# Kernel tuning notes

Hardware: AMD Instinct MI355X
Metric: run time of the kernel (lower is better)

The kernel has to match this reference:

```python
import jax, jax.numpy as jnp
import numpy as np

B, SQ, HIDDEN = 2, 2048, 2048
HEADS, GROUPS, KVC = 16, 4, 128
HPG = HEADS // GROUPS          # heads per group
LAYER_INDEX = 1
SCALE = KVC ** -0.5            # attention_softmax_scale_power = 0.5


def setup_inputs() -> dict:
    key = jax.random.key(0)
    k1, k2, k3, k4 = jax.random.split(key, 4)
    return {
        "x": jax.random.normal(k1, (B, SQ, HIDDEN), jnp.float32),
        "w_q": jax.random.normal(k2, (HIDDEN, HEADS * KVC), jnp.float32) * 0.02,
        "w_kv": jax.random.normal(k3, (HIDDEN, 2 * GROUPS * KVC), jnp.float32) * 0.02,
        "w_dense": jax.random.normal(k4, (HEADS * KVC, HIDDEN), jnp.float32) * 0.02,
    }


def reference(x, w_q, w_kv, w_dense):
    b, sq, _ = x.shape
    sk = sq
    # QKV projections
    q = jnp.einsum("bsh,he->bse", x, w_q).reshape(b, sq, GROUPS, HPG, KVC)
    kv = jnp.einsum("bsh,he->bse", x, w_kv)
    k, v = jnp.split(kv, 2, axis=-1)
    k = k.reshape(b, sk, GROUPS, KVC)
    v = v.reshape(b, sk, GROUPS, KVC)
    # scaled QK^T with the per-layer scale trick: alpha = scale/L in input
    # dtype, then cast to fp32 and multiply by L (as in _attn_fused)
    scores = jnp.einsum("bqgpd,bkgd->bgqpk", q, k) * (SCALE / LAYER_INDEX)
    scores = scores.astype(jnp.float32) * LAYER_INDEX
    # causal mask: mask = ~triu(ones, diagonal=1) -> keep where q_idx >= k_idx
    causal = (jnp.arange(sq)[:, None] >= jnp.arange(sk)[None, :])
    scores = jnp.where(causal[None, None, :, None, :], scores, -jnp.inf)
    probs = jax.nn.softmax(scores, axis=-1).astype(x.dtype)
    # dropout p = 0.0 -> no-op
    ctx = jnp.einsum("bgqpk,bkgd->bqgpd", probs, v).reshape(b, sq, HEADS * KVC)
    return jnp.einsum("bse,eh->bsh", ctx, w_dense)
```

## Files before the change

kernel.cpp:

```cpp
#include <hip/hip_runtime.h>
#include <hip/hip_bf16.h>


typedef __attribute__((ext_vector_type(4))) float f32x4;
typedef __attribute__((ext_vector_type(8))) short bf16x8;
typedef __attribute__((ext_vector_type(4))) short bf16x4;

__device__ __forceinline__ unsigned short f2bf(float f) {
    unsigned u = __builtin_bit_cast(unsigned, f);
    unsigned r = u + 0x7fffu + ((u >> 16) & 1u);
    return (unsigned short)(r >> 16);
}

__device__ __forceinline__ unsigned cvtpk_bf16(float lo, float hi) {
    unsigned r;
    asm("v_cvt_pk_bf16_f32 %0, %1, %2" : "=v"(r) : "v"(lo), "v"(hi));
    return r;
}

__device__ __forceinline__ void gl_lds16(const void* g, void* l) {
    __builtin_amdgcn_global_load_lds(
        (const __attribute__((address_space(1))) unsigned int*)g,
        (__attribute__((address_space(3))) unsigned int*)l, 16, 0, 0);
}

__device__ __forceinline__ int xcd_swizzle(int lin, int nwg) {
    return (lin & 7) * (nwg >> 3) + (lin >> 3);
}

__device__ __forceinline__ void xcvt_body(const float* __restrict__ in,
                                          unsigned short* __restrict__ out,
                                          int blk)
{
    size_t i = ((size_t)blk * 256 + threadIdx.x) * 8;
    float4 a = *reinterpret_cast<const float4*>(&in[i]);
    float4 b = *reinterpret_cast<const float4*>(&in[i + 4]);
    bf16x8 o = { (short)f2bf(a.x), (short)f2bf(a.y),
                 (short)f2bf(a.z), (short)f2bf(a.w),
                 (short)f2bf(b.x), (short)f2bf(b.y),
                 (short)f2bf(b.z), (short)f2bf(b.w) };
    *reinterpret_cast<bf16x8*>(&out[i]) = o;
}

__device__ __forceinline__ void wtrans_body(const float* __restrict__ in,
                                            unsigned short* __restrict__ out,
                                            int K, int N, int bx, int by,
                                            unsigned short* T)
{
    const int n0 = bx * 64, k0 = by * 64;
    const int tid = threadIdx.x;
#pragma unroll
    for (int i = 0; i < 4; ++i) {
        int f = tid + i * 256;
        int r = f >> 4;
        int c4 = (f & 15) * 4;
        float4 v = *reinterpret_cast<const float4*>(&in[(size_t)(k0 + r) * N + n0 + c4]);
        bf16x4 pk = { (short)f2bf(v.x), (short)f2bf(v.y),
                      (short)f2bf(v.z), (short)f2bf(v.w) };
        *reinterpret_cast<bf16x4*>(&T[r * 72 + c4]) = pk;
    }
    __syncthreads();
#pragma unroll
    for (int i = 0; i < 2; ++i) {
        int f = tid + i * 256;
        int nn = f >> 3;
        int s8 = (f & 7) * 8;
        bf16x8 o;
#pragma unroll
        for (int j = 0; j < 8; ++j) o[j] = T[(s8 + j) * 72 + nn];
        *reinterpret_cast<bf16x8*>(&out[(size_t)(n0 + nn) * K + k0 + s8]) = o;
    }
}

__device__ __forceinline__ void vtrans_body(const unsigned short* __restrict__ kv,
                                            unsigned short* __restrict__ vt,
                                            int bx, int bg, unsigned short* T)
{
    const int b = bg >> 2, g = bg & 3;
    const int s0 = bx * 64;
    const int tid = threadIdx.x;
#pragma unroll
    for (int i = 0; i < 4; ++i) {
        int f = tid + i * 256;
        int sl = f >> 4;
        int d0 = (f & 15) * 8;
        bf16x8 v = *reinterpret_cast<const bf16x8*>(
            &kv[(size_t)(b * 2048 + s0 + sl) * 1024 + 512 + g * 128 + d0]);
        bf16x4 lo = { v[0], v[1], v[2], v[3] };
        bf16x4 hi = { v[4], v[5], v[6], v[7] };
        *reinterpret_cast<bf16x4*>(&T[sl * 140 + d0])     = lo;
        *reinterpret_cast<bf16x4*>(&T[sl * 140 + d0 + 4]) = hi;
    }
    __syncthreads();
#pragma unroll
    for (int i = 0; i < 4; ++i) {
        int f = tid + i * 256;
        int d = f >> 3;
        int s8 = (f & 7) * 8;
        bf16x8 o;
#pragma unroll
        for (int j = 0; j < 8; ++j) o[j] = T[(s8 + j) * 140 + d];
        *reinterpret_cast<bf16x8*>(
            &vt[(size_t)(bg * 128 + d) * 2048 + s0 + s8]) = o;
    }
}

__global__ __launch_bounds__(256)
void prep1_kernel(const float* __restrict__ x, unsigned short* __restrict__ xbf,
                  const float* __restrict__ w_q, unsigned short* __restrict__ wqT,
                  const float* __restrict__ w_kv, unsigned short* __restrict__ wkvT)
{
    __shared__ __align__(16) unsigned short T[64 * 72];
    const int bid = blockIdx.x;
    if (bid < 4096) {
        xcvt_body(x, xbf, bid);
    } else if (bid < 4096 + 1024) {
        int r = bid - 4096;
        wtrans_body(w_q, wqT, 2048, 2048, r & 31, r >> 5, T);
    } else {
        int r = bid - 5120;
        wtrans_body(w_kv, wkvT, 2048, 1024, r & 15, r >> 4, T);
    }
}

__global__ __launch_bounds__(256)
void prep2_kernel(const float* __restrict__ w_dense, unsigned short* __restrict__ wdT,
                  const unsigned short* __restrict__ kv, unsigned short* __restrict__ vt)
{
    __shared__ __align__(16) unsigned short T[64 * 140];
    const int bid = blockIdx.x;
    if (bid < 1024) {
        wtrans_body(w_dense, wdT, 2048, 2048, bid & 31, bid >> 5, T);
    } else {
        int r = bid - 1024;
        vtrans_body(kv, vt, r & 31, r >> 5, T);
    }
}

__global__ __launch_bounds__(256)
void gemm_qkv_kernel(const unsigned short* __restrict__ A,
                     const unsigned short* __restrict__ BT,
                     void* __restrict__ C0v, void* __restrict__ C1v,
                     int M, int N, int K)
{
    __shared__ __align__(16) unsigned short Alds[3][128 * 32];
    __shared__ __align__(16) unsigned short Blds[3][128 * 32];

    const int tid = threadIdx.x;
    const int lane = tid & 63;
    const int wid = tid >> 6;
    const int wr = wid >> 1, wc = wid & 1;
    const int nbx = gridDim.x;
    const int lin = blockIdx.y * nbx + blockIdx.x;
    const int sl = xcd_swizzle(lin, nbx * gridDim.y);
    const int m0 = (sl / nbx) * 128;
    const int n0 = (sl % nbx) * 128;
    const int l16 = lane & 15, lg = lane >> 4;

    f32x4 acc[4][4];
#pragma unroll
    for (int m = 0; m < 4; ++m)
#pragma unroll
        for (int n = 0; n < 4; ++n) acc[m][n] = (f32x4){0.f, 0.f, 0.f, 0.f};

    int srow[2], skb[2];
#pragma unroll
    for (int i = 0; i < 2; ++i) {
        int L = i * 4096 + tid * 16;
        int R = L >> 7, c = L & 127;
        int cp = c ^ ((R & 7) << 4);
        srow[i] = 2 * R + (cp >> 6);
        skb[i]  = cp & 63;
    }

    auto stage = [&](int kt, int bi) {
#pragma unroll
        for (int i = 0; i < 2; ++i) {
            int L = i * 4096 + tid * 16;
            gl_lds16((const char*)A + ((size_t)(m0 + srow[i]) * K + kt) * 2 + skb[i],
                     (char*)(&Alds[bi][0]) + L);
            gl_lds16((const char*)BT + ((size_t)(n0 + srow[i]) * K + kt) * 2 + skb[i],
                     (char*)(&Blds[bi][0]) + L);
        }
    };

    const int NK = K / 32;
    stage(0, 0);
    stage(32, 1);

    for (int t = 0; t < NK; ++t) {
        const int bi = t % 3;
        if (t + 2 < NK) {
            stage((t + 2) * 32, (t + 2) % 3);
            asm volatile("s_waitcnt vmcnt(8)" ::: "memory");
        } else if (t + 1 < NK) {
            asm volatile("s_waitcnt vmcnt(4)" ::: "memory");
        } else {
            asm volatile("s_waitcnt vmcnt(0)" ::: "memory");
        }
        __builtin_amdgcn_s_barrier();

        const char* Ab = (const char*)(&Alds[bi][0]);
        const char* Bb = (const char*)(&Blds[bi][0]);

        bf16x8 af[4], bf[4];
#pragma unroll
        for (int m = 0; m < 4; ++m) {
            int row = wr * 64 + m * 16 + l16;
            int byte = (row >> 1) * 128 +
                       ((((row & 1) << 6) + lg * 16) ^ (((row >> 1) & 7) << 4));
            af[m] = *reinterpret_cast<const bf16x8*>(Ab + byte);
        }
#pragma unroll
        for (int n = 0; n < 4; ++n) {
            int row = wc * 64 + n * 16 + l16;
            int byte = (row >> 1) * 128 +
                       ((((row & 1) << 6) + lg * 16) ^ (((row >> 1) & 7) << 4));
            bf[n] = *reinterpret_cast<const bf16x8*>(Bb + byte);
        }
#pragma unroll
        for (int m = 0; m < 4; ++m)
#pragma unroll
            for (int n = 0; n < 4; ++n)
                acc[m][n] = __builtin_amdgcn_mfma_f32_16x16x32_bf16(
                    af[m], bf[n], acc[m][n], 0, 0, 0);

        __builtin_amdgcn_s_barrier();
    }

#pragma unroll
    for (int m = 0; m < 4; ++m) {
#pragma unroll
        for (int n = 0; n < 4; ++n) {
#pragma unroll
            for (int r = 0; r < 4; ++r) {
                int row = m0 + wr * 64 + m * 16 + lg * 4 + r;
                int col = n0 + wc * 64 + n * 16 + l16;
                float val = acc[m][n][r];
                if (n0 < 2048)
                    ((unsigned short*)C0v)[(size_t)row * 2048 + col] =
                        f2bf(val * 0.12751879523209208f);
                else
                    ((unsigned short*)C1v)[(size_t)row * 1024 + (col - 2048)] = f2bf(val);
            }
        }
    }
}

__global__ __launch_bounds__(256)
void gemm_dense_kernel(const unsigned short* __restrict__ A,
                       const unsigned short* __restrict__ BT,
                       float* __restrict__ C, int M, int N, int K)
{
    __shared__ __align__(16) unsigned short Alds[2][128 * 64];
    __shared__ __align__(16) unsigned short Blds[2][128 * 64];

    const int tid = threadIdx.x;
    const int lane = tid & 63;
    const int wid = tid >> 6;
    const int wr = wid >> 1, wc = wid & 1;
    const int nbx = gridDim.x;
    const int lin = blockIdx.y * nbx + blockIdx.x;
    const int sl = xcd_swizzle(lin, nbx * gridDim.y);
    const int m0 = (sl / nbx) * 128;
    const int n0 = (sl % nbx) * 128;
    const int l16 = lane & 15, lg = lane >> 4;

    f32x4 acc[4][4];
#pragma unroll
    for (int m = 0; m < 4; ++m)
#pragma unroll
        for (int n = 0; n < 4; ++n) acc[m][n] = (f32x4){0.f, 0.f, 0.f, 0.f};

    auto stage = [&](int kt, int bi) {
#pragma unroll
        for (int i = 0; i < 4; ++i) {
            int row = i * 32 + (tid >> 3);
            int cb = ((tid & 7) * 16) ^ ((row & 7) << 4);
            gl_lds16((const char*)A + ((size_t)(m0 + row) * K + kt) * 2 + cb,
                     (char*)(&Alds[bi][0]) + i * 4096 + wid * 1024);
            gl_lds16((const char*)BT + ((size_t)(n0 + row) * K + kt) * 2 + cb,
                     (char*)(&Blds[bi][0]) + i * 4096 + wid * 1024);
        }
    };

    const int NK = K / 64;
    stage(0, 0);
    int cur = 0;

    for (int kti = 0; kti < NK; ++kti) {
        if (kti + 1 < NK) {
            stage((kti + 1) * 64, cur ^ 1);
            asm volatile("s_waitcnt vmcnt(8)" ::: "memory");
        } else {
            asm volatile("s_waitcnt vmcnt(0)" ::: "memory");
        }
        __builtin_amdgcn_s_barrier();

        const char* Ab = (const char*)(&Alds[cur][0]);
        const char* Bb = (const char*)(&Blds[cur][0]);

        bf16x8 af[2][4], bf[2][4];
#pragma unroll
        for (int kd = 0; kd < 2; ++kd) {
#pragma unroll
            for (int m = 0; m < 4; ++m) {
                int row = wr * 64 + m * 16 + l16;
                af[kd][m] = *reinterpret_cast<const bf16x8*>(
                    Ab + row * 128 + ((kd * 64 + lg * 16) ^ ((row & 7) << 4)));
            }
#pragma unroll
            for (int n = 0; n < 4; ++n) {
                int row = wc * 64 + n * 16 + l16;
                bf[kd][n] = *reinterpret_cast<const bf16x8*>(
                    Bb + row * 128 + ((kd * 64 + lg * 16) ^ ((row & 7) << 4)));
            }
        }
#pragma unroll
        for (int kd = 0; kd < 2; ++kd)
#pragma unroll
            for (int m = 0; m < 4; ++m)
#pragma unroll
                for (int n = 0; n < 4; ++n)
                    acc[m][n] = __builtin_amdgcn_mfma_f32_16x16x32_bf16(
                        af[kd][m], bf[kd][n], acc[m][n], 0, 0, 0);

        __builtin_amdgcn_s_barrier();
        cur ^= 1;
    }

#pragma unroll
    for (int m = 0; m < 4; ++m) {
#pragma unroll
        for (int n = 0; n < 4; ++n) {
#pragma unroll
            for (int r = 0; r < 4; ++r) {
                int row = m0 + wr * 64 + m * 16 + lg * 4 + r;
                int col = n0 + wc * 64 + n * 16 + l16;
                C[(size_t)row * N + col] = acc[m][n][r];
            }
        }
    }
}

__global__ __launch_bounds__(256)
void attn_kernel(const unsigned short* __restrict__ Q,
                 const unsigned short* __restrict__ KV,
                 const unsigned short* __restrict__ VT,
                 unsigned short* __restrict__ CTX)
{
    constexpr int SQ = 2048;
    __shared__ __align__(16) unsigned short Klds[2][64 * 128];
    __shared__ __align__(16) unsigned short Vlds[2][128 * 64];
    __shared__ __align__(16) unsigned short Pl[4][16][64];

    const int tid = threadIdx.x;
    const int lane = tid & 63;
    const int w = tid >> 6;
    const int l16 = lane & 15, lg = lane >> 4;

    const int bid = blockIdx.x;
    const int gb = bid & 7;
    const int g = gb & 3, b = gb >> 2;
    const int pi = bid >> 3;
    const int hh = g * 4 + w;

    const size_t qbase = (size_t)b * SQ * 2048;
    const char* KVb = (const char*)KV + (size_t)b * SQ * 2048;
    const char* VTb = (const char*)VT;

    const int pswz = (l16 & 7) << 3;

    auto stage = [&](int t, int bi) {
        const int k0 = t * 64;
#pragma unroll
        for (int i = 0; i < 4; ++i) {
            int row = w * 16 + i * 4 + (lane >> 4);
            int scol = ((lane & 15) * 16) ^ ((row & 7) << 4);
            gl_lds16(KVb + (size_t)(k0 + row) * 2048 + g * 256 + scol,
                     (char*)(&Klds[bi][0]) + w * 4096 + i * 1024);
        }
#pragma unroll
        for (int i = 0; i < 4; ++i) {
            int row = w * 32 + i * 8 + (lane >> 3);
            int scol = ((lane & 7) * 16) ^ ((row & 7) << 4);
            gl_lds16(VTb + ((size_t)(gb * 128 + row) * 2048 + k0) * 2 + scol,
                     (char*)(&Vlds[bi][0]) + w * 4096 + i * 1024);
        }
    };

#pragma unroll 1
    for (int seg = 0; seg < 2; ++seg) {
        const int qt = seg ? pi : (127 - pi);
        const int ntiles = qt / 4 + 1;

        bf16x8 qfrag[4];
#pragma unroll
        for (int kd = 0; kd < 4; ++kd)
            qfrag[kd] = *reinterpret_cast<const bf16x8*>(
                &Q[qbase + (size_t)(qt * 16 + l16) * 2048 + hh * 128 + kd * 32 + lg * 8]);

        float lsum = 0.f;
        f32x4 acc[8];
#pragma unroll
        for (int nd = 0; nd < 8; ++nd) acc[nd] = (f32x4){0.f,0.f,0.f,0.f};

        stage(0, 0);

        for (int t = 0; t < ntiles; ++t) {
            const int bi = t & 1;
            const int k0 = t * 64;
            if (t + 1 < ntiles) {
                stage(t + 1, bi ^ 1);
                asm volatile("s_waitcnt vmcnt(8)" ::: "memory");
            } else {
                asm volatile("s_waitcnt vmcnt(0)" ::: "memory");
            }
            __builtin_amdgcn_s_barrier();

            const char* Kb = (const char*)(&Klds[bi][0]);
            const char* Vb = (const char*)(&Vlds[bi][0]);

            f32x4 st[4];
#pragma unroll
            for (int nf = 0; nf < 4; ++nf) st[nf] = (f32x4){0.f,0.f,0.f,0.f};
            __builtin_amdgcn_s_setprio(1);
#pragma unroll
            for (int nf = 0; nf < 4; ++nf) {
                int row = nf * 16 + l16;
#pragma unroll
                for (int kd = 0; kd < 4; ++kd) {
                    bf16x8 kf = *reinterpret_cast<const bf16x8*>(
                        Kb + row * 256 + ((kd * 64 + lg * 16) ^ ((row & 7) << 4)));
                    st[nf] = __builtin_amdgcn_mfma_f32_16x16x32_bf16(
                        kf, qfrag[kd], st[nf], 0, 0, 0);
                }
            }
            __builtin_amdgcn_s_setprio(0);

            const bool diag = (t == ntiles - 1);
            {
                float lacc = 0.f;
                const int q = qt * 16 + l16;
#pragma unroll
                for (int nf = 0; nf < 4; ++nf) {
                    float cs0 = st[nf][0];
                    float cs1 = st[nf][1];
                    float cs2 = st[nf][2];
                    float cs3 = st[nf][3];
                    if (diag) {
                        const int keyb = k0 + nf * 16 + lg * 4;
                        if (keyb + 0 > q) cs0 = -INFINITY;
                        if (keyb + 1 > q) cs1 = -INFINITY;
                        if (keyb + 2 > q) cs2 = -INFINITY;
                        if (keyb + 3 > q) cs3 = -INFINITY;
                    }
                    float p0 = exp2f(cs0), p1 = exp2f(cs1);
                    float p2 = exp2f(cs2), p3 = exp2f(cs3);
                    lacc += (p0 + p1) + (p2 + p3);
                    uint2 pk = { cvtpk_bf16(p0, p1), cvtpk_bf16(p2, p3) };
                    *reinterpret_cast<uint2*>(
                        &Pl[w][l16][(nf * 16 + lg * 4) ^ pswz]) = pk;
                }
                lacc += __shfl_xor(lacc, 16, 64);
                lacc += __shfl_xor(lacc, 32, 64);
                lsum += lacc;
            }

            __builtin_amdgcn_s_setprio(1);
#pragma unroll
            for (int kc = 0; kc < 2; ++kc) {
                bf16x8 pf = *reinterpret_cast<const bf16x8*>(
                    &Pl[w][l16][(kc * 32 + lg * 8) ^ pswz]);
#pragma unroll
                for (int nd = 0; nd < 8; ++nd) {
                    int row = nd * 16 + l16;
                    bf16x8 vf = *reinterpret_cast<const bf16x8*>(
                        Vb + row * 128 + ((kc * 64 + lg * 16) ^ ((row & 7) << 4)));
                    acc[nd] = __builtin_amdgcn_mfma_f32_16x16x32_bf16(
                        vf, pf, acc[nd], 0, 0, 0);
                }
            }
            __builtin_amdgcn_s_setprio(0);
            __builtin_amdgcn_s_barrier();
        }

        {
            float inv = 1.0f / lsum;
            const int q = qt * 16 + l16;
#pragma unroll
            for (int nd = 0; nd < 8; ++nd) {
                bf16x4 o = { (short)f2bf(acc[nd][0] * inv),
                             (short)f2bf(acc[nd][1] * inv),
                             (short)f2bf(acc[nd][2] * inv),
                             (short)f2bf(acc[nd][3] * inv) };
                *reinterpret_cast<bf16x4*>(
                    &CTX[qbase + (size_t)q * 2048 + hh * 128 + nd * 16 + lg * 4]) = o;
            }
        }
    }
}

extern "C" void kernel_launch(void* const* d_in, const int* in_sizes, int n_in,
                              void* d_out, int out_size, void* d_ws, size_t ws_size,
                              hipStream_t stream)
{
    const float* x       = (const float*)d_in[0];
    const float* w_q     = (const float*)d_in[1];
    const float* w_kv    = (const float*)d_in[2];
    const float* w_dense = (const float*)d_in[3];

    const int M = 4096;

    char* ws = (char*)d_ws;
    unsigned short* kv_buf  = (unsigned short*)(ws);
    unsigned short* ctx_buf = (unsigned short*)(ws + (8u << 20));
    unsigned short* wqT     = (unsigned short*)(ws + (24u << 20));
    unsigned short* wkvT    = (unsigned short*)(ws + (32u << 20));
    unsigned short* wdT     = wqT;
    unsigned short* xbf    = (unsigned short*)d_out;
    unsigned short* q_buf  = (unsigned short*)d_out + (size_t)M * 2048;
    unsigned short* vt_buf = (unsigned short*)d_out;

    dim3 blk(256);
    prep1_kernel<<<dim3(5632), blk, 0, stream>>>(x, xbf, w_q, wqT, w_kv, wkvT);
    gemm_qkv_kernel<<<dim3(24, 32), blk, 0, stream>>>(
        xbf, wqT, (void*)q_buf, (void*)kv_buf, M, 3072, 2048);
    prep2_kernel<<<dim3(1280), blk, 0, stream>>>(w_dense, wdT, kv_buf, vt_buf);
    attn_kernel<<<dim3(512), blk, 0, stream>>>(q_buf, kv_buf, vt_buf, ctx_buf);
    gemm_dense_kernel<<<dim3(16, 32), blk, 0, stream>>>(
        ctx_buf, wdT, (float*)d_out, M, 2048, 2048);
}
```

Baseline: 183.3 us.

## Repartition attention work: each wave owns a key slice across all four group heads

Warps now split keys and head dims instead of heads. Each wave computes scores for its 16-key slice across all 4 heads of the group, so every K fragment read from LDS feeds 4 MFMAs. Each wave then does P·V for its 32-column slice of V across all heads, through a shared P buffer. This cuts LDS traffic for K and V fragments. In exchange it adds an extra block barrier per tile, more Q registers, and a cross-wave LDS reduction of the row sums at the end.

```diff
diff --git a/kernel.cpp b/kernel.cpp
--- a/kernel.cpp
+++ b/kernel.cpp
@@ -352,7 +352,7 @@
     constexpr int SQ = 2048;
     __shared__ __align__(16) unsigned short Klds[2][64 * 128];
     __shared__ __align__(16) unsigned short Vlds[2][128 * 64];
-    __shared__ __align__(16) unsigned short Pl[4][16][64];
+    __shared__ __align__(16) unsigned short Pl[64][64];
 
     const int tid = threadIdx.x;
     const int lane = tid & 63;
@@ -363,13 +363,13 @@
     const int gb = bid & 7;
     const int g = gb & 3, b = gb >> 2;
     const int pi = bid >> 3;
-    const int hh = g * 4 + w;
 
     const size_t qbase = (size_t)b * SQ * 2048;
     const char* KVb = (const char*)KV + (size_t)b * SQ * 2048;
     const char* VTb = (const char*)VT;
 
-    const int pswz = (l16 & 7) << 3;
+    const int rsw = (l16 & 7) << 4;
+    float* Sred = reinterpret_cast<float*>(&Pl[0][0]);
 
     auto stage = [&](int t, int bi) {
         const int k0 = t * 64;
@@ -393,17 +393,23 @@
     for (int seg = 0; seg < 2; ++seg) {
         const int qt = seg ? pi : (127 - pi);
         const int ntiles = qt / 4 + 1;
-
-        bf16x8 qfrag[4];
-#pragma unroll
-        for (int kd = 0; kd < 4; ++kd)
-            qfrag[kd] = *reinterpret_cast<const bf16x8*>(
-                &Q[qbase + (size_t)(qt * 16 + l16) * 2048 + hh * 128 + kd * 32 + lg * 8]);
-
-        float lsum = 0.f;
-        f32x4 acc[8];
-#pragma unroll
-        for (int nd = 0; nd < 8; ++nd) acc[nd] = (f32x4){0.f,0.f,0.f,0.f};
+        const int q = qt * 16 + l16;
+
+        bf16x8 qfrag[4][4];
+#pragma unroll
+        for (int h = 0; h < 4; ++h)
+#pragma unroll
+            for (int kd = 0; kd < 4; ++kd)
+                qfrag[h][kd] = *reinterpret_cast<const bf16x8*>(
+                    &Q[qbase + (size_t)q * 2048 + (g * 4 + h) * 128 + kd * 32 + lg * 8]);
+
+        float part[4] = {0.f, 0.f, 0.f, 0.f};
+        f32x4 acc[4][2];
+#pragma unroll
+        for (int h = 0; h < 4; ++h) {
+            acc[h][0] = (f32x4){0.f,0.f,0.f,0.f};
+            acc[h][1] = (f32x4){0.f,0.f,0.f,0.f};
+        }
 
         stage(0, 0);
 
@@ -423,79 +429,85 @@
 
             f32x4 st[4];
 #pragma unroll
-            for (int nf = 0; nf < 4; ++nf) st[nf] = (f32x4){0.f,0.f,0.f,0.f};
+            for (int h = 0; h < 4; ++h) st[h] = (f32x4){0.f,0.f,0.f,0.f};
             __builtin_amdgcn_s_setprio(1);
 #pragma unroll
-            for (int nf = 0; nf < 4; ++nf) {
-                int row = nf * 16 + l16;
-#pragma unroll
-                for (int kd = 0; kd < 4; ++kd) {
-                    bf16x8 kf = *reinterpret_cast<const bf16x8*>(
-                        Kb + row * 256 + ((kd * 64 + lg * 16) ^ ((row & 7) << 4)));
-                    st[nf] = __builtin_amdgcn_mfma_f32_16x16x32_bf16(
-                        kf, qfrag[kd], st[nf], 0, 0, 0);
+            for (int kd = 0; kd < 4; ++kd) {
+                bf16x8 kf = *reinterpret_cast<const bf16x8*>(
+                    Kb + (w * 16 + l16) * 256 + ((kd * 64 + lg * 16) ^ rsw));
+#pragma unroll
+                for (int h = 0; h < 4; ++h)
+                    st[h] = __builtin_amdgcn_mfma_f32_16x16x32_bf16(
+                        kf, qfrag[h][kd], st[h], 0, 0, 0);
+            }
+            __builtin_amdgcn_s_setprio(0);
+
+            const bool diag = (t == ntiles - 1);
+            const int keyb = k0 + w * 16 + lg * 4;
+#pragma unroll
+            for (int h = 0; h < 4; ++h) {
+                float cs0 = st[h][0], cs1 = st[h][1];
+                float cs2 = st[h][2], cs3 = st[h][3];
+                if (diag) {
+                    if (keyb + 0 > q) cs0 = -INFINITY;
+                    if (keyb + 1 > q) cs1 = -INFINITY;
+                    if (keyb + 2 > q) cs2 = -INFINITY;
+                    if (keyb + 3 > q) cs3 = -INFINITY;
                 }
-            }
-            __builtin_amdgcn_s_setprio(0);
-
-            const bool diag = (t == ntiles - 1);
-            {
-                float lacc = 0.f;
-                const int q = qt * 16 + l16;
-#pragma unroll
-                for (int nf = 0; nf < 4; ++nf) {
-                    float cs0 = st[nf][0];
-                    float cs1 = st[nf][1];
-                    float cs2 = st[nf][2];
-                    float cs3 = st[nf][3];
-                    if (diag) {
-                        const int keyb = k0 + nf * 16 + lg * 4;
-                        if (keyb + 0 > q) cs0 = -INFINITY;
-                        if (keyb + 1 > q) cs1 = -INFINITY;
-                        if (keyb + 2 > q) cs2 = -INFINITY;
-                        if (keyb + 3 > q) cs3 = -INFINITY;
-                    }
-                    float p0 = exp2f(cs0), p1 = exp2f(cs1);
-                    float p2 = exp2f(cs2), p3 = exp2f(cs3);
-                    lacc += (p0 + p1) + (p2 + p3);
-                    uint2 pk = { cvtpk_bf16(p0, p1), cvtpk_bf16(p2, p3) };
-                    *reinterpret_cast<uint2*>(
-                        &Pl[w][l16][(nf * 16 + lg * 4) ^ pswz]) = pk;
-                }
-                lacc += __shfl_xor(lacc, 16, 64);
-                lacc += __shfl_xor(lacc, 32, 64);
-                lsum += lacc;
-            }
+                float p0 = exp2f(cs0), p1 = exp2f(cs1);
+                float p2 = exp2f(cs2), p3 = exp2f(cs3);
+                part[h] += (p0 + p1) + (p2 + p3);
+                uint2 pk = { cvtpk_bf16(p0, p1), cvtpk_bf16(p2, p3) };
+                *reinterpret_cast<uint2*>(
+                    (char*)&Pl[h * 16 + l16][0] + ((w * 32 + lg * 8) ^ rsw)) = pk;
+            }
+            asm volatile("s_waitcnt lgkmcnt(0)" ::: "memory");
+            __builtin_amdgcn_s_barrier();
 
             __builtin_amdgcn_s_setprio(1);
 #pragma unroll
             for (int kc = 0; kc < 2; ++kc) {
-                bf16x8 pf = *reinterpret_cast<const bf16x8*>(
-                    &Pl[w][l16][(kc * 32 + lg * 8) ^ pswz]);
-#pragma unroll
-                for (int nd = 0; nd < 8; ++nd) {
-                    int row = nd * 16 + l16;
-                    bf16x8 vf = *reinterpret_cast<const bf16x8*>(
-                        Vb + row * 128 + ((kc * 64 + lg * 16) ^ ((row & 7) << 4)));
-                    acc[nd] = __builtin_amdgcn_mfma_f32_16x16x32_bf16(
-                        vf, pf, acc[nd], 0, 0, 0);
+                bf16x8 vf0 = *reinterpret_cast<const bf16x8*>(
+                    Vb + (w * 32 + l16) * 128 + ((kc * 64 + lg * 16) ^ rsw));
+                bf16x8 vf1 = *reinterpret_cast<const bf16x8*>(
+                    Vb + (w * 32 + 16 + l16) * 128 + ((kc * 64 + lg * 16) ^ rsw));
+#pragma unroll
+                for (int h = 0; h < 4; ++h) {
+                    bf16x8 pf = *reinterpret_cast<const bf16x8*>(
+                        (const char*)&Pl[h * 16 + l16][0] + ((kc * 64 + lg * 16) ^ rsw));
+                    acc[h][0] = __builtin_amdgcn_mfma_f32_16x16x32_bf16(
+                        vf0, pf, acc[h][0], 0, 0, 0);
+                    acc[h][1] = __builtin_amdgcn_mfma_f32_16x16x32_bf16(
+                        vf1, pf, acc[h][1], 0, 0, 0);
                 }
             }
             __builtin_amdgcn_s_setprio(0);
             __builtin_amdgcn_s_barrier();
         }
 
-        {
-            float inv = 1.0f / lsum;
-            const int q = qt * 16 + l16;
-#pragma unroll
-            for (int nd = 0; nd < 8; ++nd) {
-                bf16x4 o = { (short)f2bf(acc[nd][0] * inv),
-                             (short)f2bf(acc[nd][1] * inv),
-                             (short)f2bf(acc[nd][2] * inv),
-                             (short)f2bf(acc[nd][3] * inv) };
+#pragma unroll
+        for (int h = 0; h < 4; ++h) {
+            part[h] += __shfl_xor(part[h], 16, 64);
+            part[h] += __shfl_xor(part[h], 32, 64);
+            Sred[(w * 4 + h) * 16 + l16] = part[h];
+        }
+        asm volatile("s_waitcnt lgkmcnt(0)" ::: "memory");
+        __builtin_amdgcn_s_barrier();
+
+#pragma unroll
+        for (int h = 0; h < 4; ++h) {
+            float ls = Sred[(0 * 4 + h) * 16 + l16] + Sred[(1 * 4 + h) * 16 + l16] +
+                       Sred[(2 * 4 + h) * 16 + l16] + Sred[(3 * 4 + h) * 16 + l16];
+            float inv = 1.0f / ls;
+#pragma unroll
+            for (int nd = 0; nd < 2; ++nd) {
+                int d0 = w * 32 + nd * 16 + lg * 4;
+                bf16x4 o = { (short)f2bf(acc[h][nd][0] * inv),
+                             (short)f2bf(acc[h][nd][1] * inv),
+                             (short)f2bf(acc[h][nd][2] * inv),
+                             (short)f2bf(acc[h][nd][3] * inv) };
                 *reinterpret_cast<bf16x4*>(
-                    &CTX[qbase + (size_t)q * 2048 + hh * 128 + nd * 16 + lg * 4]) = o;
+                    &CTX[qbase + (size_t)q * 2048 + (g * 4 + h) * 128 + d0]) = o;
             }
         }
     }
```

Result: no change. 184.0 us (+0.4%).

## Split attention into one query tile per block and drop LDS double buffering

Applied to the files above, without the earlier changes.

The attention kernel used to process two paired query tiles per block, with double-buffered K/V staging in LDS. It now launches 1024 blocks that each handle a single query tile, ordered by a zigzag mapping, and stages K/V through a single buffer with __syncthreads. launch_bounds asks for 4 blocks per SM. The goal is more parallelism and occupancy from the halved LDS footprint and extra blocks, but it gives up overlap of global loads with compute inside each block and relies on other resident blocks to hide that latency.

```diff
diff --git a/kernel.cpp b/kernel.cpp
--- a/kernel.cpp
+++ b/kernel.cpp
@@ -343,15 +343,15 @@
     }
 }
 
-__global__ __launch_bounds__(256)
+__global__ __launch_bounds__(256, 4)
 void attn_kernel(const unsigned short* __restrict__ Q,
                  const unsigned short* __restrict__ KV,
                  const unsigned short* __restrict__ VT,
                  unsigned short* __restrict__ CTX)
 {
     constexpr int SQ = 2048;
-    __shared__ __align__(16) unsigned short Klds[2][64 * 128];
-    __shared__ __align__(16) unsigned short Vlds[2][128 * 64];
+    __shared__ __align__(16) unsigned short Klds[64 * 128];
+    __shared__ __align__(16) unsigned short Vlds[128 * 64];
     __shared__ __align__(16) unsigned short Pl[4][16][64];
 
     const int tid = threadIdx.x;
@@ -362,141 +362,123 @@
     const int bid = blockIdx.x;
     const int gb = bid & 7;
     const int g = gb & 3, b = gb >> 2;
-    const int pi = bid >> 3;
+    const int j = bid >> 3;
+    const int qt = (j < 32) ? j : (j < 64) ? (95 - j) : (j < 96) ? j : (223 - j);
     const int hh = g * 4 + w;
 
     const size_t qbase = (size_t)b * SQ * 2048;
     const char* KVb = (const char*)KV + (size_t)b * SQ * 2048;
     const char* VTb = (const char*)VT;
 
+    bf16x8 qfrag[4];
+#pragma unroll
+    for (int kd = 0; kd < 4; ++kd)
+        qfrag[kd] = *reinterpret_cast<const bf16x8*>(
+            &Q[qbase + (size_t)(qt * 16 + l16) * 2048 + hh * 128 + kd * 32 + lg * 8]);
+
+    float lsum = 0.f;
+    f32x4 acc[8];
+#pragma unroll
+    for (int nd = 0; nd < 8; ++nd) acc[nd] = (f32x4){0.f,0.f,0.f,0.f};
+
+    const int ntiles = qt / 4 + 1;
     const int pswz = (l16 & 7) << 3;
 
-    auto stage = [&](int t, int bi) {
+    for (int t = 0; t < ntiles; ++t) {
         const int k0 = t * 64;
 #pragma unroll
         for (int i = 0; i < 4; ++i) {
             int row = w * 16 + i * 4 + (lane >> 4);
             int scol = ((lane & 15) * 16) ^ ((row & 7) << 4);
             gl_lds16(KVb + (size_t)(k0 + row) * 2048 + g * 256 + scol,
-                     (char*)(&Klds[bi][0]) + w * 4096 + i * 1024);
+                     (char*)Klds + w * 4096 + i * 1024);
         }
 #pragma unroll
         for (int i = 0; i < 4; ++i) {
             int row = w * 32 + i * 8 + (lane >> 3);
             int scol = ((lane & 7) * 16) ^ ((row & 7) << 4);
             gl_lds16(VTb + ((size_t)(gb * 128 + row) * 2048 + k0) * 2 + scol,
-                     (char*)(&Vlds[bi][0]) + w * 4096 + i * 1024);
-        }
-    };
-
-#pragma unroll 1
-    for (int seg = 0; seg < 2; ++seg) {
-        const int qt = seg ? pi : (127 - pi);
-        const int ntiles = qt / 4 + 1;
-
-        bf16x8 qfrag[4];
-#pragma unroll
-        for (int kd = 0; kd < 4; ++kd)
-            qfrag[kd] = *reinterpret_cast<const bf16x8*>(
-                &Q[qbase + (size_t)(qt * 16 + l16) * 2048 + hh * 128 + kd * 32 + lg * 8]);
-
-        float lsum = 0.f;
-        f32x4 acc[8];
-#pragma unroll
-        for (int nd = 0; nd < 8; ++nd) acc[nd] = (f32x4){0.f,0.f,0.f,0.f};
-
-        stage(0, 0);
-
-        for (int t = 0; t < ntiles; ++t) {
-            const int bi = t & 1;
-            const int k0 = t * 64;
-            if (t + 1 < ntiles) {
-                stage(t + 1, bi ^ 1);
-                asm volatile("s_waitcnt vmcnt(8)" ::: "memory");
-            } else {
-                asm volatile("s_waitcnt vmcnt(0)" ::: "memory");
-            }
-            __builtin_amdgcn_s_barrier();
-
-            const char* Kb = (const char*)(&Klds[bi][0]);
-            const char* Vb = (const char*)(&Vlds[bi][0]);
-
-            f32x4 st[4];
-#pragma unroll
-            for (int nf = 0; nf < 4; ++nf) st[nf] = (f32x4){0.f,0.f,0.f,0.f};
-            __builtin_amdgcn_s_setprio(1);
+                     (char*)Vlds + w * 4096 + i * 1024);
+        }
+        __syncthreads();
+
+        f32x4 st[4];
+#pragma unroll
+        for (int nf = 0; nf < 4; ++nf) st[nf] = (f32x4){0.f,0.f,0.f,0.f};
+        __builtin_amdgcn_s_setprio(1);
+#pragma unroll
+        for (int nf = 0; nf < 4; ++nf) {
+            int row = nf * 16 + l16;
+#pragma unroll
+            for (int kd = 0; kd < 4; ++kd) {
+                bf16x8 kf = *reinterpret_cast<const bf16x8*>(
+                    (const char*)Klds + row * 256 +
+                    ((kd * 64 + lg * 16) ^ ((row & 7) << 4)));
+                st[nf] = __builtin_amdgcn_mfma_f32_16x16x32_bf16(
+                    kf, qfrag[kd], st[nf], 0, 0, 0);
+            }
+        }
+        __builtin_amdgcn_s_setprio(0);
+
+        const bool diag = (t == ntiles - 1);
+        {
+            float lacc = 0.f;
+            const int q = qt * 16 + l16;
 #pragma unroll
             for (int nf = 0; nf < 4; ++nf) {
-                int row = nf * 16 + l16;
-#pragma unroll
-                for (int kd = 0; kd < 4; ++kd) {
-                    bf16x8 kf = *reinterpret_cast<const bf16x8*>(
-                        Kb + row * 256 + ((kd * 64 + lg * 16) ^ ((row & 7) << 4)));
-                    st[nf] = __builtin_amdgcn_mfma_f32_16x16x32_bf16(
-                        kf, qfrag[kd], st[nf], 0, 0, 0);
+                float cs0 = st[nf][0];
+                float cs1 = st[nf][1];
+                float cs2 = st[nf][2];
+                float cs3 = st[nf][3];
+                if (diag) {
+                    const int keyb = k0 + nf * 16 + lg * 4;
+                    if (keyb + 0 > q) cs0 = -INFINITY;
+                    if (keyb + 1 > q) cs1 = -INFINITY;
+                    if (keyb + 2 > q) cs2 = -INFINITY;
+                    if (keyb + 3 > q) cs3 = -INFINITY;
                 }
-            }
-            __builtin_amdgcn_s_setprio(0);
-
-            const bool diag = (t == ntiles - 1);
-            {
-                float lacc = 0.f;
-                const int q = qt * 16 + l16;
-#pragma unroll
-                for (int nf = 0; nf < 4; ++nf) {
-                    float cs0 = st[nf][0];
-                    float cs1 = st[nf][1];
-                    float cs2 = st[nf][2];
-                    float cs3 = st[nf][3];
-                    if (diag) {
-                        const int keyb = k0 + nf * 16 + lg * 4;
-                        if (keyb + 0 > q) cs0 = -INFINITY;
-                        if (keyb + 1 > q) cs1 = -INFINITY;
-                        if (keyb + 2 > q) cs2 = -INFINITY;
-                        if (keyb + 3 > q) cs3 = -INFINITY;
-                    }
-                    float p0 = exp2f(cs0), p1 = exp2f(cs1);
-                    float p2 = exp2f(cs2), p3 = exp2f(cs3);
-                    lacc += (p0 + p1) + (p2 + p3);
-                    uint2 pk = { cvtpk_bf16(p0, p1), cvtpk_bf16(p2, p3) };
-                    *reinterpret_cast<uint2*>(
-                        &Pl[w][l16][(nf * 16 + lg * 4) ^ pswz]) = pk;
-                }
-                lacc += __shfl_xor(lacc, 16, 64);
-                lacc += __shfl_xor(lacc, 32, 64);
-                lsum += lacc;
-            }
-
-            __builtin_amdgcn_s_setprio(1);
-#pragma unroll
-            for (int kc = 0; kc < 2; ++kc) {
-                bf16x8 pf = *reinterpret_cast<const bf16x8*>(
-                    &Pl[w][l16][(kc * 32 + lg * 8) ^ pswz]);
-#pragma unroll
-                for (int nd = 0; nd < 8; ++nd) {
-                    int row = nd * 16 + l16;
-                    bf16x8 vf = *reinterpret_cast<const bf16x8*>(
-                        Vb + row * 128 + ((kc * 64 + lg * 16) ^ ((row & 7) << 4)));
-                    acc[nd] = __builtin_amdgcn_mfma_f32_16x16x32_bf16(
-                        vf, pf, acc[nd], 0, 0, 0);
-                }
-            }
-            __builtin_amdgcn_s_setprio(0);
-            __builtin_amdgcn_s_barrier();
-        }
-
-        {
-            float inv = 1.0f / lsum;
-            const int q = qt * 16 + l16;
+                float p0 = exp2f(cs0), p1 = exp2f(cs1);
+                float p2 = exp2f(cs2), p3 = exp2f(cs3);
+                lacc += (p0 + p1) + (p2 + p3);
+                uint2 pk = { cvtpk_bf16(p0, p1), cvtpk_bf16(p2, p3) };
+                *reinterpret_cast<uint2*>(
+                    &Pl[w][l16][(nf * 16 + lg * 4) ^ pswz]) = pk;
+            }
+            lacc += __shfl_xor(lacc, 16, 64);
+            lacc += __shfl_xor(lacc, 32, 64);
+            lsum += lacc;
+        }
+
+        __builtin_amdgcn_s_setprio(1);
+#pragma unroll
+        for (int kc = 0; kc < 2; ++kc) {
+            bf16x8 pf = *reinterpret_cast<const bf16x8*>(
+                &Pl[w][l16][(kc * 32 + lg * 8) ^ pswz]);
 #pragma unroll
             for (int nd = 0; nd < 8; ++nd) {
-                bf16x4 o = { (short)f2bf(acc[nd][0] * inv),
-                             (short)f2bf(acc[nd][1] * inv),
-                             (short)f2bf(acc[nd][2] * inv),
-                             (short)f2bf(acc[nd][3] * inv) };
-                *reinterpret_cast<bf16x4*>(
-                    &CTX[qbase + (size_t)q * 2048 + hh * 128 + nd * 16 + lg * 4]) = o;
-            }
+                int row = nd * 16 + l16;
+                bf16x8 vf = *reinterpret_cast<const bf16x8*>(
+                    (const char*)Vlds + row * 128 +
+                    ((kc * 64 + lg * 16) ^ ((row & 7) << 4)));
+                acc[nd] = __builtin_amdgcn_mfma_f32_16x16x32_bf16(
+                    vf, pf, acc[nd], 0, 0, 0);
+            }
+        }
+        __builtin_amdgcn_s_setprio(0);
+        __syncthreads();
+    }
+
+    {
+        float inv = 1.0f / lsum;
+        const int q = qt * 16 + l16;
+#pragma unroll
+        for (int nd = 0; nd < 8; ++nd) {
+            bf16x4 o = { (short)f2bf(acc[nd][0] * inv),
+                         (short)f2bf(acc[nd][1] * inv),
+                         (short)f2bf(acc[nd][2] * inv),
+                         (short)f2bf(acc[nd][3] * inv) };
+            *reinterpret_cast<bf16x4*>(
+                &CTX[qbase + (size_t)q * 2048 + hh * 128 + nd * 16 + lg * 4]) = o;
         }
     }
 }
@@ -527,7 +509,7 @@
     gemm_qkv_kernel<<<dim3(24, 32), blk, 0, stream>>>(
         xbf, wqT, (void*)q_buf, (void*)kv_buf, M, 3072, 2048);
     prep2_kernel<<<dim3(1280), blk, 0, stream>>>(w_dense, wdT, kv_buf, vt_buf);
-    attn_kernel<<<dim3(512), blk, 0, stream>>>(q_buf, kv_buf, vt_buf, ctx_buf);
+    attn_kernel<<<dim3(1024), blk, 0, stream>>>(q_buf, kv_buf, vt_buf, ctx_buf);
     gemm_dense_kernel<<<dim3(16, 32), blk, 0, stream>>>(
         ctx_buf, wdT, (float*)d_out, M, 2048, 2048);
 }
```

Result: slower. 190.7 us (+4.0%).

## Retile QKV GEMM to 128x192 tiles with BK=64 double buffering

Applied to the files above, without the earlier changes.

The QKV projection GEMM moves from 128x128 output tiles with a triple-buffered BK=32 pipeline to 128x192 tiles with a double-buffered BK=64 pipeline. The grid shrinks from 768 to 512 blocks, which fills the 256 CUs in exactly two waves, and each loaded A tile is reused across more columns. The epilogue now picks the Q or KV destination per column because a tile can straddle the 2048 boundary. The cost is more accumulator registers (96 floats) and more LDS per block, which may lower occupancy, and there is one less stage of prefetch depth.

```diff
diff --git a/kernel.cpp b/kernel.cpp
--- a/kernel.cpp
+++ b/kernel.cpp
@@ -143,8 +143,8 @@
                      void* __restrict__ C0v, void* __restrict__ C1v,
                      int M, int N, int K)
 {
-    __shared__ __align__(16) unsigned short Alds[3][128 * 32];
-    __shared__ __align__(16) unsigned short Blds[3][128 * 32];
+    __shared__ __align__(16) unsigned short Alds[2][128 * 64];
+    __shared__ __align__(16) unsigned short Blds[2][192 * 64];
 
     const int tid = threadIdx.x;
     const int lane = tid & 63;
@@ -154,90 +154,87 @@
     const int lin = blockIdx.y * nbx + blockIdx.x;
     const int sl = xcd_swizzle(lin, nbx * gridDim.y);
     const int m0 = (sl / nbx) * 128;
-    const int n0 = (sl % nbx) * 128;
+    const int n0 = (sl % nbx) * 192;
     const int l16 = lane & 15, lg = lane >> 4;
 
-    f32x4 acc[4][4];
+    f32x4 acc[4][6];
 #pragma unroll
     for (int m = 0; m < 4; ++m)
 #pragma unroll
-        for (int n = 0; n < 4; ++n) acc[m][n] = (f32x4){0.f, 0.f, 0.f, 0.f};
-
-    int srow[2], skb[2];
-#pragma unroll
-    for (int i = 0; i < 2; ++i) {
-        int L = i * 4096 + tid * 16;
-        int R = L >> 7, c = L & 127;
-        int cp = c ^ ((R & 7) << 4);
-        srow[i] = 2 * R + (cp >> 6);
-        skb[i]  = cp & 63;
-    }
+        for (int n = 0; n < 6; ++n) acc[m][n] = (f32x4){0.f, 0.f, 0.f, 0.f};
 
     auto stage = [&](int kt, int bi) {
 #pragma unroll
-        for (int i = 0; i < 2; ++i) {
-            int L = i * 4096 + tid * 16;
-            gl_lds16((const char*)A + ((size_t)(m0 + srow[i]) * K + kt) * 2 + skb[i],
-                     (char*)(&Alds[bi][0]) + L);
-            gl_lds16((const char*)BT + ((size_t)(n0 + srow[i]) * K + kt) * 2 + skb[i],
-                     (char*)(&Blds[bi][0]) + L);
+        for (int i = 0; i < 4; ++i) {
+            int row = i * 32 + (tid >> 3);
+            int cb = ((tid & 7) * 16) ^ ((row & 7) << 4);
+            gl_lds16((const char*)A + ((size_t)(m0 + row) * K + kt) * 2 + cb,
+                     (char*)(&Alds[bi][0]) + i * 4096 + wid * 1024);
+        }
+#pragma unroll
+        for (int i = 0; i < 6; ++i) {
+            int row = i * 32 + (tid >> 3);
+            int cb = ((tid & 7) * 16) ^ ((row & 7) << 4);
+            gl_lds16((const char*)BT + ((size_t)(n0 + row) * K + kt) * 2 + cb,
+                     (char*)(&Blds[bi][0]) + i * 4096 + wid * 1024);
         }
     };
 
-    const int NK = K / 32;
+    const int NK = K / 64;
     stage(0, 0);
-    stage(32, 1);
-
-    for (int t = 0; t < NK; ++t) {
-        const int bi = t % 3;
-        if (t + 2 < NK) {
-            stage((t + 2) * 32, (t + 2) % 3);
-            asm volatile("s_waitcnt vmcnt(8)" ::: "memory");
-        } else if (t + 1 < NK) {
-            asm volatile("s_waitcnt vmcnt(4)" ::: "memory");
+    int cur = 0;
+
+    for (int kti = 0; kti < NK; ++kti) {
+        if (kti + 1 < NK) {
+            stage((kti + 1) * 64, cur ^ 1);
+            asm volatile("s_waitcnt vmcnt(10)" ::: "memory");
         } else {
             asm volatile("s_waitcnt vmcnt(0)" ::: "memory");
         }
         __builtin_amdgcn_s_barrier();
 
-        const char* Ab = (const char*)(&Alds[bi][0]);
-        const char* Bb = (const char*)(&Blds[bi][0]);
-
-        bf16x8 af[4], bf[4];
-#pragma unroll
-        for (int m = 0; m < 4; ++m) {
-            int row = wr * 64 + m * 16 + l16;
-            int byte = (row >> 1) * 128 +
-                       ((((row & 1) << 6) + lg * 16) ^ (((row >> 1) & 7) << 4));
-            af[m] = *reinterpret_cast<const bf16x8*>(Ab + byte);
-        }
-#pragma unroll
-        for (int n = 0; n < 4; ++n) {
-            int row = wc * 64 + n * 16 + l16;
-            int byte = (row >> 1) * 128 +
-                       ((((row & 1) << 6) + lg * 16) ^ (((row >> 1) & 7) << 4));
-            bf[n] = *reinterpret_cast<const bf16x8*>(Bb + byte);
-        }
-#pragma unroll
-        for (int m = 0; m < 4; ++m)
-#pragma unroll
-            for (int n = 0; n < 4; ++n)
-                acc[m][n] = __builtin_amdgcn_mfma_f32_16x16x32_bf16(
-                    af[m], bf[n], acc[m][n], 0, 0, 0);
+        const char* Ab = (const char*)(&Alds[cur][0]);
+        const char* Bb = (const char*)(&Blds[cur][0]);
+
+        bf16x8 af[2][4], bf[2][6];
+#pragma unroll
+        for (int kd = 0; kd < 2; ++kd) {
+#pragma unroll
+            for (int m = 0; m < 4; ++m) {
+                int row = wr * 64 + m * 16 + l16;
+                af[kd][m] = *reinterpret_cast<const bf16x8*>(
+                    Ab + row * 128 + ((kd * 64 + lg * 16) ^ ((row & 7) << 4)));
+            }
+#pragma unroll
+            for (int n = 0; n < 6; ++n) {
+                int row = wc * 96 + n * 16 + l16;
+                bf[kd][n] = *reinterpret_cast<const bf16x8*>(
+                    Bb + row * 128 + ((kd * 64 + lg * 16) ^ ((row & 7) << 4)));
+            }
+        }
+#pragma unroll
+        for (int kd = 0; kd < 2; ++kd)
+#pragma unroll
+            for (int m = 0; m < 4; ++m)
+#pragma unroll
+                for (int n = 0; n < 6; ++n)
+                    acc[m][n] = __builtin_amdgcn_mfma_f32_16x16x32_bf16(
+                        af[kd][m], bf[kd][n], acc[m][n], 0, 0, 0);
 
         __builtin_amdgcn_s_barrier();
+        cur ^= 1;
     }
 
 #pragma unroll
     for (int m = 0; m < 4; ++m) {
 #pragma unroll
-        for (int n = 0; n < 4; ++n) {
+        for (int n = 0; n < 6; ++n) {
 #pragma unroll
             for (int r = 0; r < 4; ++r) {
                 int row = m0 + wr * 64 + m * 16 + lg * 4 + r;
-                int col = n0 + wc * 64 + n * 16 + l16;
+                int col = n0 + wc * 96 + n * 16 + l16;
                 float val = acc[m][n][r];
-                if (n0 < 2048)
+                if (col < 2048)
                     ((unsigned short*)C0v)[(size_t)row * 2048 + col] =
                         f2bf(val * 0.12751879523209208f);
                 else
@@ -524,7 +521,7 @@
 
     dim3 blk(256);
     prep1_kernel<<<dim3(5632), blk, 0, stream>>>(x, xbf, w_q, wqT, w_kv, wkvT);
-    gemm_qkv_kernel<<<dim3(24, 32), blk, 0, stream>>>(
+    gemm_qkv_kernel<<<dim3(16, 32), blk, 0, stream>>>(
         xbf, wqT, (void*)q_buf, (void*)kv_buf, M, 3072, 2048);
     prep2_kernel<<<dim3(1280), blk, 0, stream>>>(w_dense, wdT, kv_buf, vt_buf);
     attn_kernel<<<dim3(512), blk, 0, stream>>>(q_buf, kv_buf, vt_buf, ctx_buf);
```

Result: faster. 172.3 us (-6.0%).
